# Performance work log

Measured on AMD Instinct MI355X. Metric: run time of the kernel, lower is better.

## Reference

```python
import math
import jax, jax.numpy as jnp
import numpy as np

N_HEAD = 12
LN_EPS = 1e-5

def _gelu(x):
    # NewGELU: tanh approximation
    c = math.sqrt(2.0 / math.pi)
    return 0.5 * x * (1.0 + jnp.tanh(c * (x + 0.044715 * x ** 3)))

def _ln(x, w, b):
    m = x.mean(-1, keepdims=True)
    v = x.var(-1, keepdims=True)
    return (x - m) / jnp.sqrt(v + LN_EPS) * w + b

def setup_inputs() -> dict:
    key = jax.random.key(0)
    ks = jax.random.split(key, 8)
    L, C, V, BS = 12, 768, 30522, 1024
    B, T = 4, 1024
    std = 0.02
    inp = {
        'idx': jax.random.randint(ks[0], (B, T), 0, V),
        'wte': jax.random.normal(ks[1], (V, C), jnp.float32) * std,
        'wpe': jax.random.normal(ks[2], (BS, C), jnp.float32) * std,
        'ln1_w': jnp.ones((L, C), jnp.float32),
        'ln1_b': jnp.zeros((L, C), jnp.float32),
        'attn_w': jax.random.normal(ks[3], (L, 3 * C, C), jnp.float32) * std,
        'attn_b': jnp.zeros((L, 3 * C), jnp.float32),
        'proj_w': jax.random.normal(ks[4], (L, C, C), jnp.float32) * (std / math.sqrt(2 * L)),
        'proj_b': jnp.zeros((L, C), jnp.float32),
        'ln2_w': jnp.ones((L, C), jnp.float32),
        'ln2_b': jnp.zeros((L, C), jnp.float32),
        'fc_w': jax.random.normal(ks[5], (L, 4 * C, C), jnp.float32) * std,
        'fc_b': jnp.zeros((L, 4 * C), jnp.float32),
        'mproj_w': jax.random.normal(ks[6], (L, C, 4 * C), jnp.float32) * (std / math.sqrt(2 * L)),
        'mproj_b': jnp.zeros((L, C), jnp.float32),
        'lnf_w': jnp.ones((C,), jnp.float32),
        'lnf_b': jnp.zeros((C,), jnp.float32),
        'lm_head_w': jax.random.normal(ks[7], (V, C), jnp.float32) * std,
    }
    return inp

def reference(idx, wte, wpe, ln1_w, ln1_b, attn_w, attn_b, proj_w, proj_b,
              ln2_w, ln2_b, fc_w, fc_b, mproj_w, mproj_b, lnf_w, lnf_b, lm_head_w):
    B, T = idx.shape
    C = wte.shape[1]
    H = N_HEAD
    D = C // H
    scale = 1.0 / math.sqrt(D)
    x = wte[idx] + wpe[:T][None]  # [B,T,C], drop is identity (p=0)

    def block(x, p):
        l1w, l1b, aw, ab, pw, pb, l2w, l2b, fw, fb, mw, mb = p
        h = _ln(x, l1w, l1b)
        qkv = jnp.einsum('btc,ec->bte', h, aw) + ab  # [B,T,3C]
        q, k, v = jnp.split(qkv, 3, axis=-1)
        q = q.reshape(B, T, H, D)
        k = k.reshape(B, T, H, D)
        v = v.reshape(B, T, H, D)
        att = jnp.einsum('bthd,bshd->bhts', q, k) * scale  # [B,H,T,T]
        att = jax.nn.softmax(att, axis=-1)  # mask=None: full attention
        y = jnp.einsum('bhts,bshd->bthd', att, v).reshape(B, T, C)
        x = x + jnp.einsum('btc,oc->bto', y, pw) + pb
        h = _gelu(jnp.einsum('btc,fc->btf', _ln(x, l2w, l2b), fw) + fb)
        x = x + jnp.einsum('btf,cf->btc', h, mw) + mb
        return x, None

    x, _ = jax.lax.scan(block, x, (ln1_w, ln1_b, attn_w, attn_b, proj_w, proj_b,
                                   ln2_w, ln2_b, fc_w, fc_b, mproj_w, mproj_b))
    x = _ln(x, lnf_w, lnf_b)
    logits = jnp.einsum('btc,vc->btv', x, lm_head_w)  # [B,T,V]
    return logits
```

## Files before the change

### kernel.cpp

```cpp
#include <hip/hip_runtime.h>
#include <hip/hip_bf16.h>
#include <math.h>

typedef __attribute__((ext_vector_type(8))) short short8;
typedef __attribute__((ext_vector_type(4))) float f32x4;

typedef unsigned short u16;

__device__ __forceinline__ u16 f2bf(float f) {
    union { float f; unsigned int u; } v; v.f = f;
    unsigned int u = v.u;
    unsigned int r = (u + 0x7fffu + ((u >> 16) & 1u)) >> 16;
    return (u16)r;
}
__device__ __forceinline__ float bf2f(u16 u) {
    union { unsigned int u; float f; } v; v.u = ((unsigned int)u) << 16;
    return v.f;
}

__device__ __forceinline__ void gload16(const void* g, void* l) {
    __builtin_amdgcn_global_load_lds(
        (const __attribute__((address_space(1))) void*)g,
        (__attribute__((address_space(3))) void*)l, 16, 0, 0);
}

__global__ __launch_bounds__(256) void castw_kernel(const float* __restrict__ src,
                                                    u16* __restrict__ dst,
                                                    long n, long npad) {
    long i = ((long)blockIdx.x * 256 + threadIdx.x) * 4;
    const long stride = (long)gridDim.x * 1024;
    for (; i < npad; i += stride) {
        ushort4 o;
        if (i < n) {
            float4 v = *reinterpret_cast<const float4*>(src + i);
            o.x = f2bf(v.x); o.y = f2bf(v.y); o.z = f2bf(v.z); o.w = f2bf(v.w);
        } else {
            o = make_ushort4(0, 0, 0, 0);
        }
        *reinterpret_cast<ushort4*>(dst + i) = o;
    }
}

__global__ __launch_bounds__(256) void embed_kernel(const int* __restrict__ idx,
                                                    const float* __restrict__ wte,
                                                    const float* __restrict__ wpe,
                                                    float* __restrict__ x) {
    const int row = blockIdx.x;
    const int tid = threadIdx.x;
    const int t = row & 1023;
    const int tok = idx[row];
    const float* we = wte + (size_t)tok * 768;
    const float* pe = wpe + (size_t)t * 768;
    float* xr = x + (size_t)row * 768;
    xr[tid]       = we[tid]       + pe[tid];
    xr[tid + 256] = we[tid + 256] + pe[tid + 256];
    xr[tid + 512] = we[tid + 512] + pe[tid + 512];
}

__global__ __launch_bounds__(256) void ln_kernel(const float* __restrict__ x,
                                                 const float* __restrict__ w,
                                                 const float* __restrict__ b,
                                                 u16* __restrict__ out) {
    const int wid = threadIdx.x >> 6, lane = threadIdx.x & 63;
    const int row = blockIdx.x * 4 + wid;
    const float* xr = x + (size_t)row * 768;
    const float4 v0 = *reinterpret_cast<const float4*>(xr + lane * 4);
    const float4 v1 = *reinterpret_cast<const float4*>(xr + 256 + lane * 4);
    const float4 v2 = *reinterpret_cast<const float4*>(xr + 512 + lane * 4);
    float s = v0.x + v0.y + v0.z + v0.w + v1.x + v1.y + v1.z + v1.w
            + v2.x + v2.y + v2.z + v2.w;
    float q = v0.x * v0.x + v0.y * v0.y + v0.z * v0.z + v0.w * v0.w
            + v1.x * v1.x + v1.y * v1.y + v1.z * v1.z + v1.w * v1.w
            + v2.x * v2.x + v2.y * v2.y + v2.z * v2.z + v2.w * v2.w;
    #pragma unroll
    for (int off = 32; off >= 1; off >>= 1) {
        s += __shfl_xor(s, off);
        q += __shfl_xor(q, off);
    }
    const float mean = s * (1.f / 768.f);
    const float var = q * (1.f / 768.f) - mean * mean;
    const float rstd = rsqrtf(var + 1e-5f);
    u16* orow = out + (size_t)row * 768;
    #pragma unroll
    for (int seg = 0; seg < 3; seg++) {
        const float4 v = seg == 0 ? v0 : (seg == 1 ? v1 : v2);
        const float4 wv = *reinterpret_cast<const float4*>(w + seg * 256 + lane * 4);
        const float4 bv = *reinterpret_cast<const float4*>(b + seg * 256 + lane * 4);
        ushort4 ov;
        ov.x = f2bf((v.x - mean) * rstd * wv.x + bv.x);
        ov.y = f2bf((v.y - mean) * rstd * wv.y + bv.y);
        ov.z = f2bf((v.z - mean) * rstd * wv.z + bv.z);
        ov.w = f2bf((v.w - mean) * rstd * wv.w + bv.w);
        *reinterpret_cast<ushort4*>(orow + seg * 256 + lane * 4) = ov;
    }
}

template<int EPI, int ORDER>
__global__ __launch_bounds__(512) void gemm_big(
        const u16* __restrict__ A, int lda,
        const u16* __restrict__ B, int ldb,
        const float* __restrict__ bias,
        void* __restrict__ Cout, int ldc,
        int N, int K, int nmt) {
    __shared__ __align__(16) u16 lds[2][384 * 32];
    const int tid = threadIdx.x;
    const int lane = tid & 63, wid = tid >> 6;
    const int nwg = gridDim.x;
    const int o = blockIdx.x;
    const int wg = (o & 7) * (nwg >> 3) + (o >> 3);
    int m0, n0;
    if (ORDER == 0) { m0 = (wg % nmt) * 256; n0 = (wg / nmt) * 128; }
    else            { n0 = (wg % nmt) * 128; m0 = (wg / nmt) * 256; }

    const int wm = (wid >> 1) * 64, wn = (wid & 1) * 64;
    const int l16 = lane & 15;
    const int qid = lane >> 4;
    const int xq8 = ((qid ^ ((l16 >> 1) & 3)) * 8);

    const int ar = tid >> 2, aq = (tid & 3) ^ ((ar >> 1) & 3);
    const size_t a_src0 = (size_t)(m0 + ar) * lda + aq * 8;
    const size_t a_src1 = (size_t)(m0 + ar + 128) * lda + aq * 8;
    const size_t b_src = (size_t)(n0 + ar) * ldb + aq * 8;

    f32x4 acc[4][4];
    #pragma unroll
    for (int i = 0; i < 4; i++)
        #pragma unroll
        for (int j = 0; j < 4; j++)
            acc[i][j] = (f32x4){0.f, 0.f, 0.f, 0.f};

    const int nk = K >> 5;
    gload16(A + a_src0, lds[0] + tid * 8);
    gload16(A + a_src1, lds[0] + tid * 8 + 4096);
    gload16(B + b_src,  lds[0] + tid * 8 + 8192);

    for (int t = 0; t < nk; ++t) {
        if (t + 1 < nk) {
            u16* buf = lds[(t + 1) & 1];
            const int k0 = (t + 1) << 5;
            gload16(A + a_src0 + k0, buf + tid * 8);
            gload16(A + a_src1 + k0, buf + tid * 8 + 4096);
            gload16(B + b_src + k0,  buf + tid * 8 + 8192);
            asm volatile("s_waitcnt vmcnt(3)" ::: "memory");
        } else {
            asm volatile("s_waitcnt vmcnt(0)" ::: "memory");
        }
        __builtin_amdgcn_s_barrier();
        asm volatile("" ::: "memory");
        const u16* As = lds[t & 1];
        const u16* Bs = lds[t & 1] + 8192;
        short8 af[4], bf[4];
        #pragma unroll
        for (int i = 0; i < 4; i++) {
            af[i] = *reinterpret_cast<const short8*>(&As[(wm + i * 16 + l16) * 32 + xq8]);
            bf[i] = *reinterpret_cast<const short8*>(&Bs[(wn + i * 16 + l16) * 32 + xq8]);
        }
        #pragma unroll
        for (int mi = 0; mi < 4; mi++)
            #pragma unroll
            for (int ni = 0; ni < 4; ni++)
                acc[mi][ni] = __builtin_amdgcn_mfma_f32_16x16x32_bf16(af[mi], bf[ni], acc[mi][ni], 0, 0, 0);
        asm volatile("" ::: "memory");
        __builtin_amdgcn_s_barrier();
    }

    if (EPI == 3) {
        float* ct = reinterpret_cast<float*>(&lds[0][0]) + wid * 1216;
        const int rw = (lane >> 4) * 4;
        const int rr = lane >> 2;
        const int rc = (lane & 3) * 16;
        #pragma unroll
        for (int mi = 0; mi < 4; mi++) {
            asm volatile("" ::: "memory");
            #pragma unroll
            for (int ni = 0; ni < 4; ni++)
                #pragma unroll
                for (int j = 0; j < 4; j++)
                    ct[(rw + j) * 76 + ni * 16 + l16] = acc[mi][ni][j];
            asm volatile("" ::: "memory");
            const int m = m0 + wm + mi * 16 + rr;
            const int nb = n0 + wn + rc;
            float* crow = (float*)Cout + (size_t)m * ldc + nb;
            #pragma unroll
            for (int q = 0; q < 4; q++) {
                const f32x4 v = *reinterpret_cast<const f32x4*>(&ct[rr * 76 + rc + q * 4]);
                if (nb + q * 4 + 3 < N) {
                    *reinterpret_cast<f32x4*>(crow + q * 4) = v;
                } else {
                    #pragma unroll
                    for (int e = 0; e < 4; e++)
                        if (nb + q * 4 + e < N) crow[q * 4 + e] = v[e];
                }
            }
            asm volatile("" ::: "memory");
            __builtin_amdgcn_s_barrier();
        }
    } else {
        const int cb = n0 + wn + l16;
        const int rb = m0 + wm + (lane >> 4) * 4;
        #pragma unroll
        for (int ni = 0; ni < 4; ni++) {
            const int n = cb + ni * 16;
            const float bv = bias[n];
            #pragma unroll
            for (int mi = 0; mi < 4; mi++) {
                #pragma unroll
                for (int j = 0; j < 4; j++) {
                    const int m = rb + mi * 16 + j;
                    float v = acc[mi][ni][j] + bv;
                    if (EPI == 0) {
                        ((u16*)Cout)[(size_t)m * ldc + n] = f2bf(v);
                    } else {
                        const float t = tanhf(0.7978845608028654f * (v + 0.044715f * v * v * v));
                        ((u16*)Cout)[(size_t)m * ldc + n] = f2bf(0.5f * v * (1.f + t));
                    }
                }
            }
        }
    }
}

__global__ __launch_bounds__(256) void gemm_splitk(
        const u16* __restrict__ A, int lda,
        const u16* __restrict__ B, int ldb,
        const float* __restrict__ bias,
        int ldc, int Kp, int nmt, int ntiles,
        float* __restrict__ resid) {
    __shared__ __align__(16) u16 lds[2][2][128 * 32];
    const int tid = threadIdx.x;
    const int lane = tid & 63, wid = tid >> 6;
    const int nwg = gridDim.x;
    const int o = blockIdx.x;
    const int wg = (o & 7) * (nwg >> 3) + (o >> 3);
    const int tile = wg % ntiles;
    const int ks = wg / ntiles;
    const int m0 = (tile % nmt) * 128, n0 = (tile / nmt) * 128;
    const int koff = ks * Kp;

    const int wm = (wid >> 1) * 64, wn = (wid & 1) * 64;
    const int l16 = lane & 15;
    const int qid = lane >> 4;
    const int xq8 = ((qid ^ ((l16 >> 1) & 3)) * 8);

    const int r0 = tid >> 2, q0 = (tid & 3) ^ ((r0 >> 1) & 3);
    const size_t a_src0 = (size_t)(m0 + r0) * lda + koff + q0 * 8;
    const size_t a_src1 = (size_t)(m0 + r0 + 64) * lda + koff + q0 * 8;
    const size_t b_src0 = (size_t)(n0 + r0) * ldb + koff + q0 * 8;
    const size_t b_src1 = (size_t)(n0 + r0 + 64) * ldb + koff + q0 * 8;

    f32x4 acc[4][4];
    #pragma unroll
    for (int i = 0; i < 4; i++)
        #pragma unroll
        for (int j = 0; j < 4; j++)
            acc[i][j] = (f32x4){0.f, 0.f, 0.f, 0.f};

    const int nk = Kp >> 5;
    gload16(A + a_src0, lds[0][0] + tid * 8);
    gload16(A + a_src1, lds[0][0] + tid * 8 + 2048);
    gload16(B + b_src0, lds[0][1] + tid * 8);
    gload16(B + b_src1, lds[0][1] + tid * 8 + 2048);

    for (int t = 0; t < nk; ++t) {
        if (t + 1 < nk) {
            u16* Ap = lds[(t + 1) & 1][0];
            u16* Bp = lds[(t + 1) & 1][1];
            const int k0 = (t + 1) << 5;
            gload16(A + a_src0 + k0, Ap + tid * 8);
            gload16(A + a_src1 + k0, Ap + tid * 8 + 2048);
            gload16(B + b_src0 + k0, Bp + tid * 8);
            gload16(B + b_src1 + k0, Bp + tid * 8 + 2048);
            asm volatile("s_waitcnt vmcnt(4)" ::: "memory");
        } else {
            asm volatile("s_waitcnt vmcnt(0)" ::: "memory");
        }
        __builtin_amdgcn_s_barrier();
        asm volatile("" ::: "memory");
        const u16* As = lds[t & 1][0];
        const u16* Bs = lds[t & 1][1];
        short8 af[4], bf[4];
        #pragma unroll
        for (int i = 0; i < 4; i++) {
            af[i] = *reinterpret_cast<const short8*>(&As[(wm + i * 16 + l16) * 32 + xq8]);
            bf[i] = *reinterpret_cast<const short8*>(&Bs[(wn + i * 16 + l16) * 32 + xq8]);
        }
        #pragma unroll
        for (int mi = 0; mi < 4; mi++)
            #pragma unroll
            for (int ni = 0; ni < 4; ni++)
                acc[mi][ni] = __builtin_amdgcn_mfma_f32_16x16x32_bf16(af[mi], bf[ni], acc[mi][ni], 0, 0, 0);
        asm volatile("" ::: "memory");
        __builtin_amdgcn_s_barrier();
    }

    const int cb = n0 + wn + l16;
    const int rb = m0 + wm + (lane >> 4) * 4;
    #pragma unroll
    for (int ni = 0; ni < 4; ni++) {
        const int n = cb + ni * 16;
        const float bv = (ks == 0) ? bias[n] : 0.f;
        #pragma unroll
        for (int mi = 0; mi < 4; mi++) {
            #pragma unroll
            for (int j = 0; j < 4; j++) {
                const int m = rb + mi * 16 + j;
                atomicAdd(&resid[(size_t)m * ldc + n], acc[mi][ni][j] + bv);
            }
        }
    }
}

template<int EPI>
__global__ __launch_bounds__(256, 2) void gemm_bt(
        const u16* __restrict__ A, int lda,
        const float* __restrict__ B, int ldb,
        const float* __restrict__ bias,
        void* __restrict__ Cout, int ldc,
        int M, int N, int K,
        float* __restrict__ resid) {
    __shared__ __align__(16) u16 As[128][40];
    __shared__ __align__(16) u16 Bs[128][40];
    const int tid = threadIdx.x;
    const int lane = tid & 63, wid = tid >> 6;
    const int m0 = blockIdx.y * 128, n0 = blockIdx.x * 128;
    const int wm = (wid >> 1) * 64, wn = (wid & 1) * 64;
    const int l16 = lane & 15, lk = (lane >> 4) * 8;

    f32x4 acc[4][4];
    #pragma unroll
    for (int i = 0; i < 4; i++)
        #pragma unroll
        for (int j = 0; j < 4; j++)
            acc[i][j] = (f32x4){0.f, 0.f, 0.f, 0.f};

    for (int k0 = 0; k0 < K; k0 += 32) {
        #pragma unroll
        for (int p = 0; p < 2; p++) {
            const int e = p * 256 + tid;
            const int r = e >> 2, c = e & 3;
            uint4 v = *reinterpret_cast<const uint4*>(A + (size_t)(m0 + r) * lda + k0 + c * 8);
            *reinterpret_cast<uint4*>(&As[r][c * 8]) = v;
        }
        #pragma unroll
        for (int p = 0; p < 4; p++) {
            const int e = p * 256 + tid;
            const int r = e >> 3, c = e & 7;
            float4 v = make_float4(0.f, 0.f, 0.f, 0.f);
            if (n0 + r < N)
                v = *reinterpret_cast<const float4*>(B + (size_t)(n0 + r) * ldb + k0 + c * 4);
            ushort4 hv;
            hv.x = f2bf(v.x); hv.y = f2bf(v.y); hv.z = f2bf(v.z); hv.w = f2bf(v.w);
            *reinterpret_cast<ushort4*>(&Bs[r][c * 4]) = hv;
        }
        __syncthreads();
        short8 af[4], bfr[4];
        #pragma unroll
        for (int i = 0; i < 4; i++) {
            af[i]  = *reinterpret_cast<const short8*>(&As[wm + i * 16 + l16][lk]);
            bfr[i] = *reinterpret_cast<const short8*>(&Bs[wn + i * 16 + l16][lk]);
        }
        #pragma unroll
        for (int mi = 0; mi < 4; mi++)
            #pragma unroll
            for (int ni = 0; ni < 4; ni++)
                acc[mi][ni] = __builtin_amdgcn_mfma_f32_16x16x32_bf16(af[mi], bfr[ni], acc[mi][ni], 0, 0, 0);
        __syncthreads();
    }

    const int cb = n0 + wn + l16;
    const int rb = m0 + wm + (lane >> 4) * 4;
    #pragma unroll
    for (int ni = 0; ni < 4; ni++) {
        const int n = cb + ni * 16;
        if (n >= N) continue;
        float bv = 0.f;
        if (EPI != 3) bv = bias[n];
        #pragma unroll
        for (int mi = 0; mi < 4; mi++) {
            #pragma unroll
            for (int j = 0; j < 4; j++) {
                const int m = rb + mi * 16 + j;
                float v = acc[mi][ni][j] + bv;
                if (EPI == 0) {
                    ((u16*)Cout)[(size_t)m * ldc + n] = f2bf(v);
                } else if (EPI == 1) {
                    resid[(size_t)m * ldc + n] += v;
                } else if (EPI == 2) {
                    const float t = tanhf(0.7978845608028654f * (v + 0.044715f * v * v * v));
                    ((u16*)Cout)[(size_t)m * ldc + n] = f2bf(0.5f * v * (1.f + t));
                } else {
                    ((float*)Cout)[(size_t)m * ldc + n] = v;
                }
            }
        }
    }
}

__global__ __launch_bounds__(512, 2) void attn_mfma_kernel(const u16* __restrict__ qkv,
                                                           u16* __restrict__ y) {
    __shared__ __align__(16) u16 Qs[128][72];
    __shared__ __align__(16) u16 Ks[2][64][72];
    __shared__ __align__(16) u16 Vt[2][64][72];
    __shared__ __align__(16) u16 Ps[8][16][72];

    const int tid = threadIdx.x;
    const int lane = tid & 63, wid = tid >> 6;
    const int l16 = lane & 15, lk = (lane >> 4) * 8;
    const int qt = blockIdx.x, h = blockIdx.y, b = blockIdx.z;

    const size_t base = (size_t)b * 1024 * 2304;
    const u16* qp = qkv + base + (size_t)(qt * 128) * 2304 + h * 64;
    const u16* kp = qkv + base + 768  + h * 64;
    const u16* vp = qkv + base + 1536 + h * 64;

    const int krr = tid >> 3, kc8 = tid & 7;
    const int vs = (tid >> 4) * 2, vdq = tid & 15;

    #pragma unroll
    for (int p = 0; p < 2; p++) {
        const int e = p * 512 + tid;
        const int rr = e >> 3, c8 = e & 7;
        *reinterpret_cast<uint4*>(&Qs[rr][c8 * 8]) =
            *reinterpret_cast<const uint4*>(qp + (size_t)rr * 2304 + c8 * 8);
    }
    uint4 kreg; ushort4 vra, vrb;
    kreg = *reinterpret_cast<const uint4*>(kp + (size_t)krr * 2304 + kc8 * 8);
    vra = *reinterpret_cast<const ushort4*>(vp + (size_t)vs * 2304 + vdq * 4);
    vrb = *reinterpret_cast<const ushort4*>(vp + (size_t)(vs + 1) * 2304 + vdq * 4);
    __syncthreads();

    short8 qf[2];
    #pragma unroll
    for (int kk = 0; kk < 2; kk++)
        qf[kk] = *reinterpret_cast<const short8*>(&Qs[wid * 16 + l16][kk * 32 + lk]);

    *reinterpret_cast<uint4*>(&Ks[0][krr][kc8 * 8]) = kreg;
    *reinterpret_cast<ushort2*>(&Vt[0][vdq * 4 + 0][vs]) = make_ushort2(vra.x, vrb.x);
    *reinterpret_cast<ushort2*>(&Vt[0][vdq * 4 + 1][vs]) = make_ushort2(vra.y, vrb.y);
    *reinterpret_cast<ushort2*>(&Vt[0][vdq * 4 + 2][vs]) = make_ushort2(vra.z, vrb.z);
    *reinterpret_cast<ushort2*>(&Vt[0][vdq * 4 + 3][vs]) = make_ushort2(vra.w, vrb.w);
    __syncthreads();

    f32x4 o_acc[4];
    #pragma unroll
    for (int i = 0; i < 4; i++) o_acc[i] = (f32x4){0.f, 0.f, 0.f, 0.f};
    float l_part[4] = {0.f, 0.f, 0.f, 0.f};

    for (int t = 0; t < 16; ++t) {
        const int cur = t & 1, nxt = cur ^ 1;
        if (t + 1 < 16) {
            const int s0 = (t + 1) * 64;
            kreg = *reinterpret_cast<const uint4*>(kp + (size_t)(s0 + krr) * 2304 + kc8 * 8);
            vra = *reinterpret_cast<const ushort4*>(vp + (size_t)(s0 + vs) * 2304 + vdq * 4);
            vrb = *reinterpret_cast<const ushort4*>(vp + (size_t)(s0 + vs + 1) * 2304 + vdq * 4);
        }

        f32x4 sa[4];
        #pragma unroll
        for (int i = 0; i < 4; i++) sa[i] = (f32x4){0.f, 0.f, 0.f, 0.f};
        #pragma unroll
        for (int nj = 0; nj < 4; nj++) {
            #pragma unroll
            for (int kk = 0; kk < 2; kk++) {
                short8 kf = *reinterpret_cast<const short8*>(&Ks[cur][nj * 16 + l16][kk * 32 + lk]);
                sa[nj] = __builtin_amdgcn_mfma_f32_16x16x32_bf16(qf[kk], kf, sa[nj], 0, 0, 0);
            }
        }
        #pragma unroll
        for (int nj = 0; nj < 4; nj++) {
            #pragma unroll
            for (int r = 0; r < 4; r++) {
                const float pv = __expf(sa[nj][r] * 0.125f);
                l_part[r] += pv;
                Ps[wid][(lane >> 4) * 4 + r][nj * 16 + l16] = f2bf(pv);
            }
        }
        short8 pa[2];
        #pragma unroll
        for (int kk = 0; kk < 2; kk++)
            pa[kk] = *reinterpret_cast<const short8*>(&Ps[wid][l16][kk * 32 + lk]);
        #pragma unroll
        for (int nd = 0; nd < 4; nd++) {
            #pragma unroll
            for (int kk = 0; kk < 2; kk++) {
                short8 vf = *reinterpret_cast<const short8*>(&Vt[cur][nd * 16 + l16][kk * 32 + lk]);
                o_acc[nd] = __builtin_amdgcn_mfma_f32_16x16x32_bf16(pa[kk], vf, o_acc[nd], 0, 0, 0);
            }
        }

        if (t + 1 < 16) {
            *reinterpret_cast<uint4*>(&Ks[nxt][krr][kc8 * 8]) = kreg;
            *reinterpret_cast<ushort2*>(&Vt[nxt][vdq * 4 + 0][vs]) = make_ushort2(vra.x, vrb.x);
            *reinterpret_cast<ushort2*>(&Vt[nxt][vdq * 4 + 1][vs]) = make_ushort2(vra.y, vrb.y);
            *reinterpret_cast<ushort2*>(&Vt[nxt][vdq * 4 + 2][vs]) = make_ushort2(vra.z, vrb.z);
            *reinterpret_cast<ushort2*>(&Vt[nxt][vdq * 4 + 3][vs]) = make_ushort2(vra.w, vrb.w);
        }
        __syncthreads();
    }

    float inv[4];
    #pragma unroll
    for (int r = 0; r < 4; r++) {
        float s = l_part[r];
        #pragma unroll
        for (int off = 8; off >= 1; off >>= 1) s += __shfl_xor(s, off);
        inv[r] = 1.f / s;
    }
    const int rowb = b * 1024 + qt * 128 + wid * 16 + (lane >> 4) * 4;
    #pragma unroll
    for (int nd = 0; nd < 4; nd++) {
        const int col = h * 64 + nd * 16 + l16;
        #pragma unroll
        for (int r = 0; r < 4; r++) {
            y[(size_t)(rowb + r) * 768 + col] = f2bf(o_acc[nd][r] * inv[r]);
        }
    }
}

extern "C" void kernel_launch(void* const* d_in, const int* in_sizes, int n_in,
                              void* d_out, int out_size, void* d_ws, size_t ws_size,
                              hipStream_t stream) {
    (void)in_sizes; (void)n_in; (void)out_size;
    const int*   idx    = (const int*)d_in[0];
    const float* wte    = (const float*)d_in[1];
    const float* wpe    = (const float*)d_in[2];
    const float* ln1w   = (const float*)d_in[3];
    const float* ln1b   = (const float*)d_in[4];
    const float* attnw  = (const float*)d_in[5];
    const float* attnb  = (const float*)d_in[6];
    const float* projw  = (const float*)d_in[7];
    const float* projb  = (const float*)d_in[8];
    const float* ln2w   = (const float*)d_in[9];
    const float* ln2b   = (const float*)d_in[10];
    const float* fcw    = (const float*)d_in[11];
    const float* fcb    = (const float*)d_in[12];
    const float* mprojw = (const float*)d_in[13];
    const float* mprojb = (const float*)d_in[14];
    const float* lnfw   = (const float*)d_in[15];
    const float* lnfb   = (const float*)d_in[16];
    const float* lmw    = (const float*)d_in[17];
    float* out = (float*)d_out;

    char* p = (char*)d_ws;
    size_t used = 0;
    auto take = [&](size_t bytes) { char* q = p + used; used += (bytes + 255) & ~(size_t)255; return q; };
    float* x      = (float*)take((size_t)4096 * 768 * 4);
    u16*   a_bf   = (u16*)take((size_t)4096 * 768 * 2);
    u16*   qkv_bf = (u16*)take((size_t)4096 * 2304 * 2);
    u16*   hid_bf = (u16*)take((size_t)4096 * 3072 * 2);
    u16*   w_lm   = (u16*)take((size_t)30592 * 768 * 2);
    const bool castLm = used <= ws_size;
    u16*   w_attn = (u16*)take((size_t)12 * 2304 * 768 * 2);
    u16*   w_proj = (u16*)take((size_t)12 * 768 * 768 * 2);
    u16*   w_fc   = (u16*)take((size_t)12 * 3072 * 768 * 2);
    u16*   w_mprj = (u16*)take((size_t)12 * 768 * 3072 * 2);
    const bool castAll = used <= ws_size;

    embed_kernel<<<4096, 256, 0, stream>>>(idx, wte, wpe, x);

    if (castLm)
        castw_kernel<<<2048, 256, 0, stream>>>(lmw, w_lm, (long)30522 * 768, (long)30592 * 768);
    if (castAll) {
        castw_kernel<<<2048, 256, 0, stream>>>(attnw,  w_attn, (long)12 * 2304 * 768, (long)12 * 2304 * 768);
        castw_kernel<<<2048, 256, 0, stream>>>(projw,  w_proj, (long)12 * 768 * 768,  (long)12 * 768 * 768);
        castw_kernel<<<2048, 256, 0, stream>>>(fcw,    w_fc,   (long)12 * 3072 * 768, (long)12 * 3072 * 768);
        castw_kernel<<<2048, 256, 0, stream>>>(mprojw, w_mprj, (long)12 * 768 * 3072, (long)12 * 768 * 3072);
    }

    for (int l = 0; l < 12; l++) {
        ln_kernel<<<1024, 256, 0, stream>>>(x, ln1w + l * 768, ln1b + l * 768, a_bf);
        if (castAll) {
            gemm_big<0, 0><<<16 * 18, 512, 0, stream>>>(
                a_bf, 768, w_attn + (size_t)l * 2304 * 768, 768, attnb + l * 2304,
                (void*)qkv_bf, 2304, 2304, 768, 16);
        } else {
            gemm_bt<0><<<dim3(18, 32), 256, 0, stream>>>(
                a_bf, 768, attnw + (size_t)l * 2304 * 768, 768, attnb + l * 2304,
                (void*)qkv_bf, 2304, 4096, 2304, 768, nullptr);
        }
        attn_mfma_kernel<<<dim3(8, 12, 4), 512, 0, stream>>>(qkv_bf, a_bf);
        if (castAll) {
            gemm_splitk<<<192 * 2, 256, 0, stream>>>(
                a_bf, 768, w_proj + (size_t)l * 768 * 768, 768, projb + l * 768,
                768, 384, 32, 192, x);
        } else {
            gemm_bt<1><<<dim3(6, 32), 256, 0, stream>>>(
                a_bf, 768, projw + (size_t)l * 768 * 768, 768, projb + l * 768,
                nullptr, 768, 4096, 768, 768, x);
        }
        ln_kernel<<<1024, 256, 0, stream>>>(x, ln2w + l * 768, ln2b + l * 768, a_bf);
        if (castAll) {
            gemm_big<2, 0><<<16 * 24, 512, 0, stream>>>(
                a_bf, 768, w_fc + (size_t)l * 3072 * 768, 768, fcb + l * 3072,
                (void*)hid_bf, 3072, 3072, 768, 16);
            gemm_splitk<<<192 * 4, 256, 0, stream>>>(
                hid_bf, 3072, w_mprj + (size_t)l * 768 * 3072, 3072, mprojb + l * 768,
                768, 768, 32, 192, x);
        } else {
            gemm_bt<2><<<dim3(24, 32), 256, 0, stream>>>(
                a_bf, 768, fcw + (size_t)l * 3072 * 768, 768, fcb + l * 3072,
                (void*)hid_bf, 3072, 4096, 3072, 768, nullptr);
            gemm_bt<1><<<dim3(6, 32), 256, 0, stream>>>(
                hid_bf, 3072, mprojw + (size_t)l * 768 * 3072, 3072, mprojb + l * 768,
                nullptr, 768, 4096, 768, 3072, x);
        }
    }

    ln_kernel<<<1024, 256, 0, stream>>>(x, lnfw, lnfb, a_bf);
    if (castLm) {
        gemm_big<3, 1><<<16 * 239, 512, 0, stream>>>(
            a_bf, 768, w_lm, 768, nullptr, (void*)out, 30522, 30522, 768, 239);
    } else {
        gemm_bt<3><<<dim3(239, 32), 256, 0, stream>>>(
            a_bf, 768, lmw, 768, nullptr, (void*)out, 30522, 4096, 30522, 768, nullptr);
    }
}
```

Before: 2.996 ms.

## Replace split-K atomic GEMMs with 128x64 full-K tiles; reorder LM-head tile mapping

```diff
diff --git a/kernel.cpp b/kernel.cpp
--- a/kernel.cpp
+++ b/kernel.cpp
@@ -95,7 +95,7 @@
     }
 }
 
-template<int EPI, int ORDER>
+template<int EPI, int ORDER, int SWZ>
 __global__ __launch_bounds__(512) void gemm_big(
         const u16* __restrict__ A, int lda,
         const u16* __restrict__ B, int ldb,
@@ -107,7 +107,7 @@
     const int lane = tid & 63, wid = tid >> 6;
     const int nwg = gridDim.x;
     const int o = blockIdx.x;
-    const int wg = (o & 7) * (nwg >> 3) + (o >> 3);
+    const int wg = SWZ ? ((o & 7) * (nwg >> 3) + (o >> 3)) : o;
     int m0, n0;
     if (ORDER == 0) { m0 = (wg % nmt) * 256; n0 = (wg / nmt) * 128; }
     else            { n0 = (wg % nmt) * 128; m0 = (wg / nmt) * 256; }
@@ -220,74 +220,68 @@
     }
 }
 
-__global__ __launch_bounds__(256) void gemm_splitk(
+__global__ __launch_bounds__(256) void gemm_half(
         const u16* __restrict__ A, int lda,
         const u16* __restrict__ B, int ldb,
         const float* __restrict__ bias,
-        int ldc, int Kp, int nmt, int ntiles,
+        int ldc, int K, int nmt,
         float* __restrict__ resid) {
-    __shared__ __align__(16) u16 lds[2][2][128 * 32];
+    __shared__ __align__(16) u16 lds[2][192 * 32];
     const int tid = threadIdx.x;
     const int lane = tid & 63, wid = tid >> 6;
     const int nwg = gridDim.x;
     const int o = blockIdx.x;
     const int wg = (o & 7) * (nwg >> 3) + (o >> 3);
-    const int tile = wg % ntiles;
-    const int ks = wg / ntiles;
-    const int m0 = (tile % nmt) * 128, n0 = (tile / nmt) * 128;
-    const int koff = ks * Kp;
-
-    const int wm = (wid >> 1) * 64, wn = (wid & 1) * 64;
+    const int m0 = (wg % nmt) * 128, n0 = (wg / nmt) * 64;
+
+    const int wm = (wid >> 1) * 64, wn = (wid & 1) * 32;
     const int l16 = lane & 15;
     const int qid = lane >> 4;
     const int xq8 = ((qid ^ ((l16 >> 1) & 3)) * 8);
 
-    const int r0 = tid >> 2, q0 = (tid & 3) ^ ((r0 >> 1) & 3);
-    const size_t a_src0 = (size_t)(m0 + r0) * lda + koff + q0 * 8;
-    const size_t a_src1 = (size_t)(m0 + r0 + 64) * lda + koff + q0 * 8;
-    const size_t b_src0 = (size_t)(n0 + r0) * ldb + koff + q0 * 8;
-    const size_t b_src1 = (size_t)(n0 + r0 + 64) * ldb + koff + q0 * 8;
-
-    f32x4 acc[4][4];
+    const int ar = tid >> 2, aq = (tid & 3) ^ ((ar >> 1) & 3);
+    const size_t a_src0 = (size_t)(m0 + ar) * lda + aq * 8;
+    const size_t a_src1 = (size_t)(m0 + ar + 64) * lda + aq * 8;
+    const size_t b_src = (size_t)(n0 + (tid >> 2)) * ldb + aq * 8;
+
+    f32x4 acc[4][2];
     #pragma unroll
     for (int i = 0; i < 4; i++)
         #pragma unroll
-        for (int j = 0; j < 4; j++)
+        for (int j = 0; j < 2; j++)
             acc[i][j] = (f32x4){0.f, 0.f, 0.f, 0.f};
 
-    const int nk = Kp >> 5;
-    gload16(A + a_src0, lds[0][0] + tid * 8);
-    gload16(A + a_src1, lds[0][0] + tid * 8 + 2048);
-    gload16(B + b_src0, lds[0][1] + tid * 8);
-    gload16(B + b_src1, lds[0][1] + tid * 8 + 2048);
+    const int nk = K >> 5;
+    gload16(A + a_src0, lds[0] + tid * 8);
+    gload16(A + a_src1, lds[0] + tid * 8 + 2048);
+    gload16(B + b_src,  lds[0] + tid * 8 + 4096);
 
     for (int t = 0; t < nk; ++t) {
         if (t + 1 < nk) {
-            u16* Ap = lds[(t + 1) & 1][0];
-            u16* Bp = lds[(t + 1) & 1][1];
+            u16* buf = lds[(t + 1) & 1];
             const int k0 = (t + 1) << 5;
-            gload16(A + a_src0 + k0, Ap + tid * 8);
-            gload16(A + a_src1 + k0, Ap + tid * 8 + 2048);
-            gload16(B + b_src0 + k0, Bp + tid * 8);
-            gload16(B + b_src1 + k0, Bp + tid * 8 + 2048);
-            asm volatile("s_waitcnt vmcnt(4)" ::: "memory");
+            gload16(A + a_src0 + k0, buf + tid * 8);
+            gload16(A + a_src1 + k0, buf + tid * 8 + 2048);
+            gload16(B + b_src + k0,  buf + tid * 8 + 4096);
+            asm volatile("s_waitcnt vmcnt(3)" ::: "memory");
         } else {
             asm volatile("s_waitcnt vmcnt(0)" ::: "memory");
         }
         __builtin_amdgcn_s_barrier();
         asm volatile("" ::: "memory");
-        const u16* As = lds[t & 1][0];
-        const u16* Bs = lds[t & 1][1];
-        short8 af[4], bf[4];
-        #pragma unroll
-        for (int i = 0; i < 4; i++) {
+        const u16* As = lds[t & 1];
+        const u16* Bs = lds[t & 1] + 4096;
+        short8 af[4], bf[2];
+        #pragma unroll
+        for (int i = 0; i < 4; i++)
             af[i] = *reinterpret_cast<const short8*>(&As[(wm + i * 16 + l16) * 32 + xq8]);
-            bf[i] = *reinterpret_cast<const short8*>(&Bs[(wn + i * 16 + l16) * 32 + xq8]);
-        }
+        #pragma unroll
+        for (int j = 0; j < 2; j++)
+            bf[j] = *reinterpret_cast<const short8*>(&Bs[(wn + j * 16 + l16) * 32 + xq8]);
         #pragma unroll
         for (int mi = 0; mi < 4; mi++)
             #pragma unroll
-            for (int ni = 0; ni < 4; ni++)
+            for (int ni = 0; ni < 2; ni++)
                 acc[mi][ni] = __builtin_amdgcn_mfma_f32_16x16x32_bf16(af[mi], bf[ni], acc[mi][ni], 0, 0, 0);
         asm volatile("" ::: "memory");
         __builtin_amdgcn_s_barrier();
@@ -296,15 +290,15 @@
     const int cb = n0 + wn + l16;
     const int rb = m0 + wm + (lane >> 4) * 4;
     #pragma unroll
-    for (int ni = 0; ni < 4; ni++) {
+    for (int ni = 0; ni < 2; ni++) {
         const int n = cb + ni * 16;
-        const float bv = (ks == 0) ? bias[n] : 0.f;
+        const float bv = bias[n];
         #pragma unroll
         for (int mi = 0; mi < 4; mi++) {
             #pragma unroll
             for (int j = 0; j < 4; j++) {
                 const int m = rb + mi * 16 + j;
-                atomicAdd(&resid[(size_t)m * ldc + n], acc[mi][ni][j] + bv);
+                resid[(size_t)m * ldc + n] += acc[mi][ni][j] + bv;
             }
         }
     }
@@ -570,7 +564,7 @@
     for (int l = 0; l < 12; l++) {
         ln_kernel<<<1024, 256, 0, stream>>>(x, ln1w + l * 768, ln1b + l * 768, a_bf);
         if (castAll) {
-            gemm_big<0, 0><<<16 * 18, 512, 0, stream>>>(
+            gemm_big<0, 0, 1><<<16 * 18, 512, 0, stream>>>(
                 a_bf, 768, w_attn + (size_t)l * 2304 * 768, 768, attnb + l * 2304,
                 (void*)qkv_bf, 2304, 2304, 768, 16);
         } else {
@@ -580,9 +574,9 @@
         }
         attn_mfma_kernel<<<dim3(8, 12, 4), 512, 0, stream>>>(qkv_bf, a_bf);
         if (castAll) {
-            gemm_splitk<<<192 * 2, 256, 0, stream>>>(
+            gemm_half<<<32 * 12, 256, 0, stream>>>(
                 a_bf, 768, w_proj + (size_t)l * 768 * 768, 768, projb + l * 768,
-                768, 384, 32, 192, x);
+                768, 768, 32, x);
         } else {
             gemm_bt<1><<<dim3(6, 32), 256, 0, stream>>>(
                 a_bf, 768, projw + (size_t)l * 768 * 768, 768, projb + l * 768,
@@ -590,12 +584,12 @@
         }
         ln_kernel<<<1024, 256, 0, stream>>>(x, ln2w + l * 768, ln2b + l * 768, a_bf);
         if (castAll) {
-            gemm_big<2, 0><<<16 * 24, 512, 0, stream>>>(
+            gemm_big<2, 0, 1><<<16 * 24, 512, 0, stream>>>(
                 a_bf, 768, w_fc + (size_t)l * 3072 * 768, 768, fcb + l * 3072,
                 (void*)hid_bf, 3072, 3072, 768, 16);
-            gemm_splitk<<<192 * 4, 256, 0, stream>>>(
+            gemm_half<<<32 * 12, 256, 0, stream>>>(
                 hid_bf, 3072, w_mprj + (size_t)l * 768 * 3072, 3072, mprojb + l * 768,
-                768, 768, 32, 192, x);
+                768, 3072, 32, x);
         } else {
             gemm_bt<2><<<dim3(24, 32), 256, 0, stream>>>(
                 a_bf, 768, fcw + (size_t)l * 3072 * 768, 768, fcb + l * 3072,
@@ -608,8 +602,8 @@
 
     ln_kernel<<<1024, 256, 0, stream>>>(x, lnfw, lnfb, a_bf);
     if (castLm) {
-        gemm_big<3, 1><<<16 * 239, 512, 0, stream>>>(
-            a_bf, 768, w_lm, 768, nullptr, (void*)out, 30522, 30522, 768, 239);
+        gemm_big<3, 0, 0><<<16 * 239, 512, 0, stream>>>(
+            a_bf, 768, w_lm, 768, nullptr, (void*)out, 30522, 30522, 768, 16);
     } else {
         gemm_bt<3><<<dim3(239, 32), 256, 0, stream>>>(
             a_bf, 768, lmw, 768, nullptr, (void*)out, 30522, 4096, 30522, 768, nullptr);
```

Result: faster. 2.723 ms (-9.1%).
